# Optimization experiments

Hardware: AMD Instinct MI355X
Metric: run time of the kernel (lower is better)

Reference implementation:

```python
import jax, jax.numpy as jnp
import numpy as np

B, N, F, DEG = 64, 1024, 128, 8
K1, K2, K3 = 512, 256, 128  # ceil(0.5*N) cascaded pool sizes
NUM_CLASSES = 10
E = B * N * DEG

def _elu(x):
    return jnp.where(x > 0, x, jnp.expm1(x))

def gcn(x, W, b, src, dst, ev, n):
    # PyG GCNConv with improved=True: self-loop weight 2, symmetric norm
    h = x @ W
    w = ev.astype(h.dtype)
    deg = jax.ops.segment_sum(w, dst, num_segments=n) + 2.0
    dinv = jax.lax.rsqrt(deg)
    coef = (w * dinv[src] * dinv[dst])[:, None]
    out = jax.ops.segment_sum(h[src] * coef, dst, num_segments=n)
    out = out + h * (2.0 * dinv * dinv)[:, None]  # self-loop term
    return out + b

def topk_pool(x, p, src, dst, ev, bg, npg, k):
    # score = tanh(x.p/||p||); keep top-k per graph; mask+remap edges
    score = jnp.tanh((x @ p) / jnp.linalg.norm(p))
    vals, idx = jax.lax.top_k(score.reshape(bg, npg), k)
    perm = (idx + (jnp.arange(bg) * npg)[:, None]).reshape(-1)
    x_new = x[perm] * vals.reshape(-1)[:, None]
    remap = jnp.full((bg * npg,), -1, jnp.int32).at[perm].set(
        jnp.arange(bg * k, dtype=jnp.int32))
    s2, d2 = remap[src], remap[dst]
    ev2 = ev & (s2 >= 0) & (d2 >= 0)
    return x_new, jnp.maximum(s2, 0), jnp.maximum(d2, 0), ev2, perm

def setup_inputs() -> dict:
    key = jax.random.key(0)
    ks = jax.random.split(key, 16)
    offs = (jnp.arange(B) * N)[:, None]
    e_per = DEG * N
    src = (jax.random.randint(ks[0], (B, e_per), 0, N) + offs).reshape(-1).astype(jnp.int32)
    dst = (jax.random.randint(ks[1], (B, e_per), 0, N) + offs).reshape(-1).astype(jnp.int32)
    def w(k, shape, fan_in):
        return jax.random.normal(k, shape, jnp.float32) / np.sqrt(fan_in)
    return {
        "x": jax.random.normal(ks[2], (B * N, F), jnp.float32),
        "W1": w(ks[3], (F, 32), F), "b1": jnp.zeros((32,)), "p1": w(ks[4], (32,), 32),
        "W2": w(ks[5], (32, 64), 32), "b2": jnp.zeros((64,)), "p2": w(ks[6], (64,), 64),
        "W3": w(ks[7], (64, 128), 64), "b3": jnp.zeros((128,)), "p3": w(ks[8], (128,), 128),
        "W4": w(ks[9], (128, 256), 128), "b4": jnp.zeros((256,)),
        "W5": w(ks[10], (384, 128), 384), "b5": jnp.zeros((128,)),
        "W6": w(ks[11], (192, 64), 192), "b6": jnp.zeros((64,)),
        "W7": w(ks[12], (96, 32), 96), "b7": jnp.zeros((32,)),
        "Wl": w(ks[13], (64, 64), 64),
        "Wc": w(ks[14], (64, NUM_CLASSES), 64), "bc": jnp.zeros((NUM_CLASSES,)),
        "src": src, "dst": dst,
    }

def reference(x, W1, b1, p1, W2, b2, p2, W3, b3, p3, W4, b4,
              W5, b5, W6, b6, W7, b7, Wl, Wc, bc, src, dst):
    ev0 = jnp.ones((E,), bool)
    x1 = _elu(gcn(x, W1, b1, src, dst, ev0, B * N))
    x2, s2, d2, ev2, idx2 = topk_pool(x1, p1, src, dst, ev0, B, N, K1)
    x2 = _elu(x2)
    x3 = _elu(gcn(x2, W2, b2, s2, d2, ev2, B * K1))
    x4, s4, d4, ev4, idx4 = topk_pool(x3, p2, s2, d2, ev2, B, K1, K2)
    x4 = _elu(x4)
    x5 = _elu(gcn(x4, W3, b3, s4, d4, ev4, B * K2))
    x6, s6, d6, ev6, idx6 = topk_pool(x5, p3, s4, d4, ev4, B, K2, K3)
    x6 = _elu(x6)
    x7 = _elu(gcn(x6, W4, b4, s6, d6, ev6, B * K3))
    x8 = jnp.zeros((B * K2, 256), x7.dtype).at[idx6].set(x7)
    x8 = _elu(jnp.concatenate([x8, x5], axis=1))
    x9 = _elu(gcn(x8, W5, b5, s4, d4, ev4, B * K2))
    x10 = jnp.zeros((B * K1, 128), x9.dtype).at[idx4].set(x9)
    x10 = _elu(jnp.concatenate([x10, x3], axis=1))
    x11 = _elu(gcn(x10, W6, b6, s2, d2, ev2, B * K1))
    x12 = jnp.zeros((B * N, 64), x11.dtype).at[idx2].set(x11)
    x12 = _elu(jnp.concatenate([x12, x1], axis=1))
    x13 = _elu(gcn(x12, W7, b7, src, dst, ev0, B * N))
    batch = jnp.repeat(jnp.arange(B), N)
    gmp = jax.ops.segment_max(x13, batch, num_segments=B)
    gap = jax.ops.segment_sum(x13, batch, num_segments=B) / N
    g = _elu(jnp.concatenate([gmp, gap], axis=1))
    g = _elu(g @ Wl)
    logits = g @ Wc + bc
    return jax.nn.log_softmax(logits, axis=-1)
```

## Files before the change

kernel.cpp:

```cpp
#include <hip/hip_runtime.h>
#include <hip/hip_bf16.h>
#include <math.h>

#define B_ 64
#define N_ 1024
#define E_ 524288
#define K1_ 512
#define K2_ 256
#define K3_ 128
#define M0_ 65536
#define M1_ 32768
#define M2_ 16384
#define M3_ 8192

static __device__ __forceinline__ float eluf(float x){ return x > 0.f ? x : expm1f(x); }
static __device__ __forceinline__ float4 elu4(float4 v){
  float4 o; o.x=eluf(v.x); o.y=eluf(v.y); o.z=eluf(v.z); o.w=eluf(v.w); return o;
}

template<int BM,int BN,int MODE>
__global__ __launch_bounds__(256) void k_mm(const float* __restrict__ X,
    const float* __restrict__ W, float* __restrict__ H, int M, int K, int N,
    const int* __restrict__ perm, const float* __restrict__ vals,
    const float* __restrict__ Xd, const int* __restrict__ orig,
    const int* __restrict__ rm, int WD4){
  constexpr int TX = BN/4;
  constexpr int TY = 256/TX;
  constexpr int RM = BM/TY;
  __shared__ float Xs[BM][36];
  __shared__ float Ws[32][BN];
  const int t = threadIdx.x;
  const int tx = t % TX, ty = t / TX;
  const int m0 = blockIdx.x*BM, n0 = blockIdx.y*BN;
  float acc[RM][4];
  #pragma unroll
  for (int r=0;r<RM;++r){acc[r][0]=0.f;acc[r][1]=0.f;acc[r][2]=0.f;acc[r][3]=0.f;}
  for (int k0=0;k0<K;k0+=32){
    #pragma unroll
    for (int l=0;l<BM/32;++l){
      int fi=l*256+t, row=fi>>3, q=fi&7;
      int m = m0+row;
      int c4 = (k0>>2)+q;
      float4 v;
      if (MODE==0){
        v = *(const float4*)(X + (size_t)m*K + (c4<<2));
      } else if (MODE==1){
        int pm = perm[m]; float vv = vals[m];
        float4 h = *(const float4*)(X + (size_t)pm*K + (c4<<2));
        v.x=eluf(h.x*vv); v.y=eluf(h.y*vv); v.z=eluf(h.z*vv); v.w=eluf(h.w*vv);
      } else {
        if (c4 < WD4){
          int o = orig ? orig[m] : m;
          int j = rm[o];
          if (j>=0) v = elu4(*(const float4*)(Xd + ((size_t)j*WD4 + c4)*4));
          else { v.x=0.f;v.y=0.f;v.z=0.f;v.w=0.f; }
        } else {
          int ws4 = (K>>2) - WD4;
          v = elu4(*(const float4*)(X + ((size_t)m*ws4 + (c4-WD4))*4));
        }
      }
      *(float4*)(&Xs[row][q*4]) = v;
    }
    #pragma unroll
    for (int l=0;l<BN/32;++l){
      int fi=l*256+t, wrow=fi/(BN/4), wq=fi%(BN/4);
      *(float4*)(&Ws[wrow][wq*4]) = *(const float4*)(W + (size_t)(k0+wrow)*N + n0 + wq*4);
    }
    __syncthreads();
    #pragma unroll
    for (int kq=0;kq<32;kq+=4){
      float4 xv[RM];
      #pragma unroll
      for (int r=0;r<RM;++r) xv[r] = *(const float4*)(&Xs[ty*RM+r][kq]);
      #pragma unroll
      for (int j=0;j<4;++j){
        float4 wv = *(const float4*)(&Ws[kq+j][tx*4]);
        #pragma unroll
        for (int r=0;r<RM;++r){
          float xs = (j==0)?xv[r].x:(j==1)?xv[r].y:(j==2)?xv[r].z:xv[r].w;
          acc[r][0]=fmaf(xs,wv.x,acc[r][0]);
          acc[r][1]=fmaf(xs,wv.y,acc[r][1]);
          acc[r][2]=fmaf(xs,wv.z,acc[r][2]);
          acc[r][3]=fmaf(xs,wv.w,acc[r][3]);
        }
      }
    }
    __syncthreads();
  }
  #pragma unroll
  for (int r=0;r<RM;++r){
    int m = m0 + ty*RM + r;
    float4 h; h.x=acc[r][0];h.y=acc[r][1];h.z=acc[r][2];h.w=acc[r][3];
    *(float4*)(H + (size_t)m*N + n0 + tx*4) = h;
  }
}

__global__ void k_deg0(const int* __restrict__ dst, int* __restrict__ degi){
  int i = blockIdx.x*256+threadIdx.x; if (i>=E_) return;
  atomicAdd(&degi[dst[i]], 1);
}
__global__ void k_place0(const int* __restrict__ src, const int* __restrict__ dst,
                         int* __restrict__ cursor, int* __restrict__ col){
  int i = blockIdx.x*256+threadIdx.x; if (i>=E_) return;
  int p = atomicAdd(&cursor[dst[i]], 1);
  col[p] = src[i];
}

__global__ __launch_bounds__(256) void k_scanA(const int* __restrict__ degi,
                                               int* __restrict__ bsum){
  __shared__ int ls[256];
  int b = blockIdx.x, t = threadIdx.x;
  ls[t] = degi[b*256+t]; __syncthreads();
  for (int o=128;o>0;o>>=1){ if (t<o) ls[t]+=ls[t+o]; __syncthreads(); }
  if (t==0) bsum[b] = ls[0];
}
__global__ __launch_bounds__(256) void k_scanB(int* __restrict__ bsum){
  __shared__ int ps[256];
  int t = threadIdx.x;
  ps[t] = bsum[t]; __syncthreads();
  for (int o=1;o<256;o<<=1){
    int v = (t>=o) ? ps[t-o] : 0;
    __syncthreads(); ps[t]+=v; __syncthreads();
  }
  bsum[t] = ps[t];
}
__global__ __launch_bounds__(256) void k_scanC(const int* __restrict__ degi,
    const int* __restrict__ bsum, int* __restrict__ rowptr,
    int* __restrict__ cursor, float* __restrict__ dinv){
  __shared__ int ps[256];
  int b = blockIdx.x, t = threadIdx.x;
  int i = b*256+t;
  int d = degi[i];
  ps[t] = d; __syncthreads();
  for (int o=1;o<256;o<<=1){
    int v = (t>=o) ? ps[t-o] : 0;
    __syncthreads(); ps[t]+=v; __syncthreads();
  }
  int off = (b==0 ? 0 : bsum[b-1]) + ps[t] - d;
  rowptr[i] = off; cursor[i] = off;
  dinv[i] = rsqrtf((float)d + 2.f);
  if (i == M0_-1) rowptr[M0_] = off + d;
}

__global__ void k_deg_orig(const int* __restrict__ orig, const int* __restrict__ rowptr0,
                           const int* __restrict__ col0, const int* __restrict__ rm,
                           float* __restrict__ dinv, int M){
  int i = blockIdx.x*256+threadIdx.x; if (i>=M) return;
  int o = orig[i];
  int beg = rowptr0[o], end = rowptr0[o+1];
  int d = 0;
  for (int j=beg;j<end;++j) d += (rm[col0[j]] >= 0) ? 1 : 0;
  dinv[i] = rsqrtf((float)d + 2.f);
}

__global__ void k_compose_idx(const int* __restrict__ prevOrig, const int* __restrict__ idxL,
                              int* __restrict__ origL, int n){
  int i = blockIdx.x*256+threadIdx.x; if (i<n) origL[i] = prevOrig[idxL[i]];
}

template<int F, bool SCORE>
__global__ __launch_bounds__(256) void k_gather(const int* __restrict__ rowptr,
    const int* __restrict__ col, const float* __restrict__ dinv,
    const float* __restrict__ H, const float* __restrict__ bias,
    float* __restrict__ OUT, int M,
    const float* __restrict__ p, float* __restrict__ score){
  constexpr int FQ = F/4;
  int i = blockIdx.x*256+threadIdx.x;
  if (i >= M*FQ) return;
  int n = i/FQ, q = i - (i/FQ)*FQ;
  int beg = rowptr[n], end = rowptr[n+1];
  float4 acc; acc.x=0.f;acc.y=0.f;acc.z=0.f;acc.w=0.f;
  for (int j=beg;j<end;++j){
    int s = col[j];
    float c = dinv[s];
    float4 h = *(const float4*)(H + (size_t)s*F + q*4);
    acc.x=fmaf(c,h.x,acc.x); acc.y=fmaf(c,h.y,acc.y);
    acc.z=fmaf(c,h.z,acc.z); acc.w=fmaf(c,h.w,acc.w);
  }
  float dn = dinv[n];
  float sc = 2.f*dn*dn;
  float4 hn = *(const float4*)(H + (size_t)n*F + q*4);
  float4 bv = *(const float4*)(bias + q*4);
  float4 o;
  o.x = eluf(fmaf(sc,hn.x,fmaf(dn,acc.x,bv.x)));
  o.y = eluf(fmaf(sc,hn.y,fmaf(dn,acc.y,bv.y)));
  o.z = eluf(fmaf(sc,hn.z,fmaf(dn,acc.z,bv.z)));
  o.w = eluf(fmaf(sc,hn.w,fmaf(dn,acc.w,bv.w)));
  *(float4*)(OUT + (size_t)n*F + q*4) = o;
  if (SCORE){
    float4 pv = *(const float4*)(p + q*4);
    float dot = o.x*pv.x + o.y*pv.y + o.z*pv.z + o.w*pv.w;
    float n2  = pv.x*pv.x + pv.y*pv.y + pv.z*pv.z + pv.w*pv.w;
    #pragma unroll
    for (int mk=FQ>>1; mk>0; mk>>=1){
      dot += __shfl_xor(dot, mk);
      n2  += __shfl_xor(n2,  mk);
    }
    if (q==0) score[n] = tanhf(dot * rsqrtf(n2));
  }
}

template<int F, bool SCORE>
__global__ __launch_bounds__(256) void k_gather_rm(const int* __restrict__ orig,
    const int* __restrict__ rowptr0, const int* __restrict__ col0,
    const int* __restrict__ rm, const float* __restrict__ dinv,
    const float* __restrict__ H, const float* __restrict__ bias,
    float* __restrict__ OUT, int M,
    const float* __restrict__ p, float* __restrict__ score){
  constexpr int FQ = F/4;
  int i = blockIdx.x*256+threadIdx.x;
  if (i >= M*FQ) return;
  int n = i/FQ, q = i - (i/FQ)*FQ;
  int o = orig[n];
  int beg = rowptr0[o], end = rowptr0[o+1];
  float4 acc; acc.x=0.f;acc.y=0.f;acc.z=0.f;acc.w=0.f;
  for (int j=beg;j<end;++j){
    int s = rm[col0[j]];
    if (s >= 0){
      float c = dinv[s];
      float4 h = *(const float4*)(H + (size_t)s*F + q*4);
      acc.x=fmaf(c,h.x,acc.x); acc.y=fmaf(c,h.y,acc.y);
      acc.z=fmaf(c,h.z,acc.z); acc.w=fmaf(c,h.w,acc.w);
    }
  }
  float dn = dinv[n];
  float sc = 2.f*dn*dn;
  float4 hn = *(const float4*)(H + (size_t)n*F + q*4);
  float4 bv = *(const float4*)(bias + q*4);
  float4 ov;
  ov.x = eluf(fmaf(sc,hn.x,fmaf(dn,acc.x,bv.x)));
  ov.y = eluf(fmaf(sc,hn.y,fmaf(dn,acc.y,bv.y)));
  ov.z = eluf(fmaf(sc,hn.z,fmaf(dn,acc.z,bv.z)));
  ov.w = eluf(fmaf(sc,hn.w,fmaf(dn,acc.w,bv.w)));
  *(float4*)(OUT + (size_t)n*F + q*4) = ov;
  if (SCORE){
    float4 pv = *(const float4*)(p + q*4);
    float dot = ov.x*pv.x + ov.y*pv.y + ov.z*pv.z + ov.w*pv.w;
    float n2  = pv.x*pv.x + pv.y*pv.y + pv.z*pv.z + pv.w*pv.w;
    #pragma unroll
    for (int mk=FQ>>1; mk>0; mk>>=1){
      dot += __shfl_xor(dot, mk);
      n2  += __shfl_xor(n2,  mk);
    }
    if (q==0) score[n] = tanhf(dot * rsqrtf(n2));
  }
}

__global__ void k_topk(const float* __restrict__ score, int npg, int K,
                       int* __restrict__ perm, float* __restrict__ vals){
  __shared__ float ss[1024]; __shared__ int si[1024];
  int g = blockIdx.x, tid = threadIdx.x;
  ss[tid] = score[g*npg + tid]; si[tid] = tid;
  __syncthreads();
  for (int k=2;k<=npg;k<<=1){
    for (int j=k>>1;j>0;j>>=1){
      int ixj = tid ^ j;
      if (ixj > tid){
        float s1=ss[tid], s2=ss[ixj]; int i1=si[tid], i2=si[ixj];
        bool aAfterB = (s1 < s2) || (s1==s2 && i1 > i2);
        bool sw = ((tid & k)==0) ? aAfterB : !aAfterB;
        if (sw){ ss[tid]=s2; si[tid]=i2; ss[ixj]=s1; si[ixj]=i1; }
      }
      __syncthreads();
    }
  }
  if (tid < K){ perm[g*K+tid] = g*npg + si[tid]; vals[g*K+tid] = ss[tid]; }
}

__global__ void k_remap_set(const int* __restrict__ perm, int* __restrict__ remap, int n){
  int i = blockIdx.x*256+threadIdx.x; if (i<n) remap[perm[i]] = i;
}

__global__ void k_head(const float* __restrict__ x13, const float* __restrict__ Wl,
                       const float* __restrict__ Wc, const float* __restrict__ bc,
                       float* __restrict__ out){
  __shared__ float smax[256], ssum[256];
  __shared__ float gv[64], g2[64], logit[10];
  int g = blockIdx.x, t = threadIdx.x;
  int f = t & 31, r0 = t >> 5;
  float mx = -3.4e38f, sm = 0.f;
  const float* base = x13 + (size_t)g*N_*32;
  for (int r=r0; r<N_; r+=8){ float v = base[r*32+f]; mx = fmaxf(mx,v); sm += v; }
  smax[t]=mx; ssum[t]=sm; __syncthreads();
  if (t<128){ smax[t]=fmaxf(smax[t],smax[t+128]); ssum[t]+=ssum[t+128]; } __syncthreads();
  if (t<64){ smax[t]=fmaxf(smax[t],smax[t+64]); ssum[t]+=ssum[t+64]; } __syncthreads();
  if (t<32){
    float m2 = fmaxf(smax[t],smax[t+32]); float s2 = ssum[t]+ssum[t+32];
    gv[t] = eluf(m2); gv[32+t] = eluf(s2 * (1.f/N_));
  }
  __syncthreads();
  if (t<64){
    float acc=0.f;
    #pragma unroll
    for (int i2=0;i2<64;++i2) acc = fmaf(gv[i2], Wl[i2*64+t], acc);
    g2[t] = eluf(acc);
  }
  __syncthreads();
  if (t<10){
    float acc = bc[t];
    #pragma unroll
    for (int j=0;j<64;++j) acc = fmaf(g2[j], Wc[j*10+t], acc);
    logit[t] = acc;
  }
  __syncthreads();
  if (t==0){
    float m=-3.4e38f; for (int c=0;c<10;++c) m=fmaxf(m,logit[c]);
    float s=0.f; for (int c=0;c<10;++c) s += expf(logit[c]-m);
    float lse = m + logf(s);
    for (int c=0;c<10;++c) out[g*10+c] = logit[c]-lse;
  }
}

extern "C" void kernel_launch(void* const* d_in, const int* in_sizes, int n_in,
                              void* d_out, int out_size, void* d_ws, size_t ws_size,
                              hipStream_t stream){
  const float* x  = (const float*)d_in[0];
  const float* W1 = (const float*)d_in[1];
  const float* b1 = (const float*)d_in[2];
  const float* p1 = (const float*)d_in[3];
  const float* W2 = (const float*)d_in[4];
  const float* b2 = (const float*)d_in[5];
  const float* p2 = (const float*)d_in[6];
  const float* W3 = (const float*)d_in[7];
  const float* b3 = (const float*)d_in[8];
  const float* p3 = (const float*)d_in[9];
  const float* W4 = (const float*)d_in[10];
  const float* b4 = (const float*)d_in[11];
  const float* W5 = (const float*)d_in[12];
  const float* b5 = (const float*)d_in[13];
  const float* W6 = (const float*)d_in[14];
  const float* b6 = (const float*)d_in[15];
  const float* W7 = (const float*)d_in[16];
  const float* b7 = (const float*)d_in[17];
  const float* Wl = (const float*)d_in[18];
  const float* Wc = (const float*)d_in[19];
  const float* bc = (const float*)d_in[20];
  const int* src0 = (const int*)d_in[21];
  const int* dst0 = (const int*)d_in[22];
  float* out = (float*)d_out;

  char* wsp = (char*)d_ws;
  size_t off = 0;
  auto alloc = [&](size_t bytes)->char*{
    char* p = wsp + off;
    off += (bytes + 255) & ~(size_t)255;
    return p;
  };
  float* bufA = (float*)alloc((size_t)2097152*4);
  float* bufB = (float*)alloc((size_t)2097152*4);
  float* bufC = (float*)alloc((size_t)2097152*4);
  float* bufD = (float*)alloc((size_t)2097152*4);
  float* bufH = (float*)alloc((size_t)2097152*4);
  float* score= (float*)alloc((size_t)M0_*4);
  float* vals2= (float*)alloc((size_t)M1_*4);
  float* vals4= (float*)alloc((size_t)M2_*4);
  float* vals6= (float*)alloc((size_t)M3_*4);
  int* idx2 = (int*)alloc((size_t)M1_*4);
  int* idx4 = (int*)alloc((size_t)M2_*4);
  int* idx6 = (int*)alloc((size_t)M3_*4);
  int* orig4 = (int*)alloc((size_t)M2_*4);
  int* orig6 = (int*)alloc((size_t)M3_*4);
  int* rm02 = (int*)alloc((size_t)M0_*4);
  int* rm04 = (int*)alloc((size_t)M0_*4);
  int* rm06 = (int*)alloc((size_t)M0_*4);
  int* col0 = (int*)alloc((size_t)E_*4);
  int* rowptr0 = (int*)alloc((size_t)(M0_+1)*4);
  int* cursor0 = (int*)alloc((size_t)M0_*4);
  int* degi0 = (int*)alloc((size_t)M0_*4);
  int* bsum  = (int*)alloc((size_t)256*4);
  float* dinv0 = (float*)alloc((size_t)M0_*4);
  float* dinv2 = (float*)alloc((size_t)M1_*4);
  float* dinv4 = (float*)alloc((size_t)M2_*4);
  float* dinv6 = (float*)alloc((size_t)M3_*4);

  auto NB = [](int total){ return (total+255)/256; };

  hipMemsetAsync(degi0, 0, (size_t)M0_*4, stream);
  k_deg0<<<NB(E_),256,0,stream>>>(dst0, degi0);
  k_scanA<<<256,256,0,stream>>>(degi0, bsum);
  k_scanB<<<1,256,0,stream>>>(bsum);
  k_scanC<<<256,256,0,stream>>>(degi0, bsum, rowptr0, cursor0, dinv0);
  k_place0<<<NB(E_),256,0,stream>>>(src0, dst0, cursor0, col0);

  k_mm<128,32,0><<<dim3(M0_/128,1),256,0,stream>>>(x, W1, bufH, M0_, 128, 32,
      nullptr,nullptr,nullptr,nullptr,nullptr,0);
  k_gather<32,true><<<NB(M0_*8),256,0,stream>>>(rowptr0, col0, dinv0, bufH, b1, bufA, M0_, p1, score);

  k_topk<<<B_,1024,0,stream>>>(score, 1024, K1_, idx2, vals2);
  hipMemsetAsync(rm02, 0xFF, (size_t)M0_*4, stream);
  k_remap_set<<<NB(M1_),256,0,stream>>>(idx2, rm02, M1_);
  k_deg_orig<<<NB(M1_),256,0,stream>>>(idx2, rowptr0, col0, rm02, dinv2, M1_);

  k_mm<64,64,1><<<dim3(M1_/64,1),256,0,stream>>>(bufA, W2, bufH, M1_, 32, 64,
      idx2, vals2, nullptr,nullptr,nullptr,0);
  k_gather_rm<64,true><<<NB(M1_*16),256,0,stream>>>(idx2, rowptr0, col0, rm02, dinv2, bufH, b2, bufB, M1_, p2, score);

  k_topk<<<B_,512,0,stream>>>(score, 512, K2_, idx4, vals4);
  k_compose_idx<<<NB(M2_),256,0,stream>>>(idx2, idx4, orig4, M2_);
  hipMemsetAsync(rm04, 0xFF, (size_t)M0_*4, stream);
  k_remap_set<<<NB(M2_),256,0,stream>>>(orig4, rm04, M2_);
  k_deg_orig<<<NB(M2_),256,0,stream>>>(orig4, rowptr0, col0, rm04, dinv4, M2_);

  k_mm<64,64,1><<<dim3(M2_/64,2),256,0,stream>>>(bufB, W3, bufH, M2_, 64, 128,
      idx4, vals4, nullptr,nullptr,nullptr,0);
  k_gather_rm<128,true><<<NB(M2_*32),256,0,stream>>>(orig4, rowptr0, col0, rm04, dinv4, bufH, b3, bufC, M2_, p3, score);

  k_topk<<<B_,256,0,stream>>>(score, 256, K3_, idx6, vals6);
  k_compose_idx<<<NB(M3_),256,0,stream>>>(orig4, idx6, orig6, M3_);
  hipMemsetAsync(rm06, 0xFF, (size_t)M0_*4, stream);
  k_remap_set<<<NB(M3_),256,0,stream>>>(orig6, rm06, M3_);
  k_deg_orig<<<NB(M3_),256,0,stream>>>(orig6, rowptr0, col0, rm06, dinv6, M3_);

  k_mm<64,64,1><<<dim3(M3_/64,4),256,0,stream>>>(bufC, W4, bufH, M3_, 128, 256,
      idx6, vals6, nullptr,nullptr,nullptr,0);
  k_gather_rm<256,false><<<NB(M3_*64),256,0,stream>>>(orig6, rowptr0, col0, rm06, dinv6, bufH, b4, bufD, M3_, nullptr, nullptr);

  k_mm<64,64,2><<<dim3(M2_/64,2),256,0,stream>>>(bufC, W5, bufH, M2_, 384, 128,
      nullptr,nullptr, bufD, orig4, rm06, 64);
  k_gather_rm<128,false><<<NB(M2_*32),256,0,stream>>>(orig4, rowptr0, col0, rm04, dinv4, bufH, b5, bufD, M2_, nullptr, nullptr);

  k_mm<64,64,2><<<dim3(M1_/64,1),256,0,stream>>>(bufB, W6, bufH, M1_, 192, 64,
      nullptr,nullptr, bufD, idx2, rm04, 32);
  k_gather_rm<64,false><<<NB(M1_*16),256,0,stream>>>(idx2, rowptr0, col0, rm02, dinv2, bufH, b6, bufC, M1_, nullptr, nullptr);

  k_mm<128,32,2><<<dim3(M0_/128,1),256,0,stream>>>(bufA, W7, bufH, M0_, 96, 32,
      nullptr,nullptr, bufC, nullptr, rm02, 16);
  k_gather<32,false><<<NB(M0_*8),256,0,stream>>>(rowptr0, col0, dinv0, bufH, b7, bufA, M0_, nullptr, nullptr);

  k_head<<<B_,256,0,stream>>>(bufA, Wl, Wc, bc, out);

  (void)in_sizes; (void)n_in; (void)out_size; (void)ws_size;
}
```

Before: 403.9 us.

## Build CSR per graph in one kernel and fuse top-k pooling bookkeeping

Replaces the global degree-count, three-pass scan and edge-placement kernels with a single per-graph kernel that counts degrees, scans and places edges using shared-memory atomics. This relies on edges being grouped by graph in contiguous blocks of 8192. It also fuses top-k sorting, index composition, remap reset and set, and pooled degree computation into one kernel per pooling level. The aim is to remove many small kernel launches, memsets and global atomics. In exchange the CSR and pooling work run on only 64 blocks, and correctness depends on the edge-ordering assumption and on the remap writes being visible within each block.

```diff
diff --git a/kernel.cpp b/kernel.cpp
--- a/kernel.cpp
+++ b/kernel.cpp
@@ -5,6 +5,7 @@
 #define B_ 64
 #define N_ 1024
 #define E_ 524288
+#define EPG_ 8192
 #define K1_ 512
 #define K2_ 256
 #define K3_ 128
@@ -95,67 +96,81 @@
   }
 }
 
-__global__ void k_deg0(const int* __restrict__ dst, int* __restrict__ degi){
-  int i = blockIdx.x*256+threadIdx.x; if (i>=E_) return;
-  atomicAdd(&degi[dst[i]], 1);
-}
-__global__ void k_place0(const int* __restrict__ src, const int* __restrict__ dst,
-                         int* __restrict__ cursor, int* __restrict__ col){
-  int i = blockIdx.x*256+threadIdx.x; if (i>=E_) return;
-  int p = atomicAdd(&cursor[dst[i]], 1);
-  col[p] = src[i];
-}
-
-__global__ __launch_bounds__(256) void k_scanA(const int* __restrict__ degi,
-                                               int* __restrict__ bsum){
-  __shared__ int ls[256];
-  int b = blockIdx.x, t = threadIdx.x;
-  ls[t] = degi[b*256+t]; __syncthreads();
-  for (int o=128;o>0;o>>=1){ if (t<o) ls[t]+=ls[t+o]; __syncthreads(); }
-  if (t==0) bsum[b] = ls[0];
-}
-__global__ __launch_bounds__(256) void k_scanB(int* __restrict__ bsum){
-  __shared__ int ps[256];
-  int t = threadIdx.x;
-  ps[t] = bsum[t]; __syncthreads();
-  for (int o=1;o<256;o<<=1){
+__global__ __launch_bounds__(1024) void k_csr(const int* __restrict__ src0,
+    const int* __restrict__ dst0, int* __restrict__ rowptr,
+    int* __restrict__ col, float* __restrict__ dinv){
+  __shared__ int ldeg[1024];
+  __shared__ int ps[1024];
+  __shared__ int lcur[1024];
+  const int g = blockIdx.x, t = threadIdx.x;
+  const int ebase = g*EPG_, nbase = g<<10;
+  ldeg[t] = 0;
+  __syncthreads();
+  #pragma unroll
+  for (int i=0;i<EPG_/1024;++i){
+    int e = ebase + i*1024 + t;
+    atomicAdd(&ldeg[dst0[e] - nbase], 1);
+  }
+  __syncthreads();
+  int d = ldeg[t];
+  ps[t] = d; __syncthreads();
+  for (int o=1;o<1024;o<<=1){
     int v = (t>=o) ? ps[t-o] : 0;
-    __syncthreads(); ps[t]+=v; __syncthreads();
-  }
-  bsum[t] = ps[t];
-}
-__global__ __launch_bounds__(256) void k_scanC(const int* __restrict__ degi,
-    const int* __restrict__ bsum, int* __restrict__ rowptr,
-    int* __restrict__ cursor, float* __restrict__ dinv){
-  __shared__ int ps[256];
-  int b = blockIdx.x, t = threadIdx.x;
-  int i = b*256+t;
-  int d = degi[i];
-  ps[t] = d; __syncthreads();
-  for (int o=1;o<256;o<<=1){
-    int v = (t>=o) ? ps[t-o] : 0;
-    __syncthreads(); ps[t]+=v; __syncthreads();
-  }
-  int off = (b==0 ? 0 : bsum[b-1]) + ps[t] - d;
-  rowptr[i] = off; cursor[i] = off;
-  dinv[i] = rsqrtf((float)d + 2.f);
-  if (i == M0_-1) rowptr[M0_] = off + d;
-}
-
-__global__ void k_deg_orig(const int* __restrict__ orig, const int* __restrict__ rowptr0,
-                           const int* __restrict__ col0, const int* __restrict__ rm,
-                           float* __restrict__ dinv, int M){
-  int i = blockIdx.x*256+threadIdx.x; if (i>=M) return;
-  int o = orig[i];
-  int beg = rowptr0[o], end = rowptr0[o+1];
-  int d = 0;
-  for (int j=beg;j<end;++j) d += (rm[col0[j]] >= 0) ? 1 : 0;
-  dinv[i] = rsqrtf((float)d + 2.f);
-}
-
-__global__ void k_compose_idx(const int* __restrict__ prevOrig, const int* __restrict__ idxL,
-                              int* __restrict__ origL, int n){
-  int i = blockIdx.x*256+threadIdx.x; if (i<n) origL[i] = prevOrig[idxL[i]];
+    __syncthreads(); ps[t] += v; __syncthreads();
+  }
+  int excl = ps[t] - d;
+  rowptr[nbase + t] = ebase + excl;
+  lcur[t] = excl;
+  dinv[nbase + t] = rsqrtf((float)d + 2.f);
+  if (g == B_-1 && t == 1023) rowptr[M0_] = E_;
+  __syncthreads();
+  #pragma unroll
+  for (int i=0;i<EPG_/1024;++i){
+    int e = ebase + i*1024 + t;
+    int dl = dst0[e] - nbase;
+    int p = atomicAdd(&lcur[dl], 1);
+    col[ebase + p] = src0[e];
+  }
+}
+
+__global__ __launch_bounds__(1024) void k_pool(const float* __restrict__ score,
+    int npg, int K, const int* __restrict__ prevOrig,
+    const int* __restrict__ rowptr0, const int* __restrict__ col0,
+    int* __restrict__ perm, float* __restrict__ vals,
+    int* __restrict__ orig, int* __restrict__ rm, float* __restrict__ dinv){
+  __shared__ float ss[1024]; __shared__ int si[1024];
+  const int g = blockIdx.x, t = threadIdx.x;
+  for (int i=t; i<1024; i+=npg) rm[(g<<10)+i] = -1;
+  ss[t] = score[g*npg + t]; si[t] = t;
+  __syncthreads();
+  for (int k=2;k<=npg;k<<=1){
+    for (int j=k>>1;j>0;j>>=1){
+      int ixj = t ^ j;
+      if (ixj > t){
+        float s1=ss[t], s2=ss[ixj]; int i1=si[t], i2=si[ixj];
+        bool aAfterB = (s1 < s2) || (s1==s2 && i1 > i2);
+        bool sw = ((t & k)==0) ? aAfterB : !aAfterB;
+        if (sw){ ss[t]=s2; si[t]=i2; ss[ixj]=s1; si[ixj]=i1; }
+      }
+      __syncthreads();
+    }
+  }
+  int o = -1;
+  if (t < K){
+    int pl = g*npg + si[t];
+    perm[g*K+t] = pl;
+    vals[g*K+t] = ss[t];
+    o = prevOrig ? prevOrig[pl] : pl;
+    orig[g*K+t] = o;
+    rm[o] = g*K + t;
+  }
+  __syncthreads();
+  if (t < K){
+    int beg = rowptr0[o], end = rowptr0[o+1];
+    int d = 0;
+    for (int j=beg;j<end;++j) d += (rm[col0[j]] >= 0) ? 1 : 0;
+    dinv[g*K+t] = rsqrtf((float)d + 2.f);
+  }
 }
 
 template<int F, bool SCORE>
@@ -244,31 +259,6 @@
     }
     if (q==0) score[n] = tanhf(dot * rsqrtf(n2));
   }
-}
-
-__global__ void k_topk(const float* __restrict__ score, int npg, int K,
-                       int* __restrict__ perm, float* __restrict__ vals){
-  __shared__ float ss[1024]; __shared__ int si[1024];
-  int g = blockIdx.x, tid = threadIdx.x;
-  ss[tid] = score[g*npg + tid]; si[tid] = tid;
-  __syncthreads();
-  for (int k=2;k<=npg;k<<=1){
-    for (int j=k>>1;j>0;j>>=1){
-      int ixj = tid ^ j;
-      if (ixj > tid){
-        float s1=ss[tid], s2=ss[ixj]; int i1=si[tid], i2=si[ixj];
-        bool aAfterB = (s1 < s2) || (s1==s2 && i1 > i2);
-        bool sw = ((tid & k)==0) ? aAfterB : !aAfterB;
-        if (sw){ ss[tid]=s2; si[tid]=i2; ss[ixj]=s1; si[ixj]=i1; }
-      }
-      __syncthreads();
-    }
-  }
-  if (tid < K){ perm[g*K+tid] = g*npg + si[tid]; vals[g*K+tid] = ss[tid]; }
-}
-
-__global__ void k_remap_set(const int* __restrict__ perm, int* __restrict__ remap, int n){
-  int i = blockIdx.x*256+threadIdx.x; if (i<n) remap[perm[i]] = i;
 }
 
 __global__ void k_head(const float* __restrict__ x13, const float* __restrict__ Wl,
@@ -365,9 +355,6 @@
   int* rm06 = (int*)alloc((size_t)M0_*4);
   int* col0 = (int*)alloc((size_t)E_*4);
   int* rowptr0 = (int*)alloc((size_t)(M0_+1)*4);
-  int* cursor0 = (int*)alloc((size_t)M0_*4);
-  int* degi0 = (int*)alloc((size_t)M0_*4);
-  int* bsum  = (int*)alloc((size_t)256*4);
   float* dinv0 = (float*)alloc((size_t)M0_*4);
   float* dinv2 = (float*)alloc((size_t)M1_*4);
   float* dinv4 = (float*)alloc((size_t)M2_*4);
@@ -375,41 +362,28 @@
 
   auto NB = [](int total){ return (total+255)/256; };
 
-  hipMemsetAsync(degi0, 0, (size_t)M0_*4, stream);
-  k_deg0<<<NB(E_),256,0,stream>>>(dst0, degi0);
-  k_scanA<<<256,256,0,stream>>>(degi0, bsum);
-  k_scanB<<<1,256,0,stream>>>(bsum);
-  k_scanC<<<256,256,0,stream>>>(degi0, bsum, rowptr0, cursor0, dinv0);
-  k_place0<<<NB(E_),256,0,stream>>>(src0, dst0, cursor0, col0);
+  k_csr<<<B_,1024,0,stream>>>(src0, dst0, rowptr0, col0, dinv0);
 
   k_mm<128,32,0><<<dim3(M0_/128,1),256,0,stream>>>(x, W1, bufH, M0_, 128, 32,
       nullptr,nullptr,nullptr,nullptr,nullptr,0);
   k_gather<32,true><<<NB(M0_*8),256,0,stream>>>(rowptr0, col0, dinv0, bufH, b1, bufA, M0_, p1, score);
 
-  k_topk<<<B_,1024,0,stream>>>(score, 1024, K1_, idx2, vals2);
-  hipMemsetAsync(rm02, 0xFF, (size_t)M0_*4, stream);
-  k_remap_set<<<NB(M1_),256,0,stream>>>(idx2, rm02, M1_);
-  k_deg_orig<<<NB(M1_),256,0,stream>>>(idx2, rowptr0, col0, rm02, dinv2, M1_);
+  k_pool<<<B_,1024,0,stream>>>(score, 1024, K1_, nullptr, rowptr0, col0,
+      idx2, vals2, idx2, rm02, dinv2);
 
   k_mm<64,64,1><<<dim3(M1_/64,1),256,0,stream>>>(bufA, W2, bufH, M1_, 32, 64,
       idx2, vals2, nullptr,nullptr,nullptr,0);
   k_gather_rm<64,true><<<NB(M1_*16),256,0,stream>>>(idx2, rowptr0, col0, rm02, dinv2, bufH, b2, bufB, M1_, p2, score);
 
-  k_topk<<<B_,512,0,stream>>>(score, 512, K2_, idx4, vals4);
-  k_compose_idx<<<NB(M2_),256,0,stream>>>(idx2, idx4, orig4, M2_);
-  hipMemsetAsync(rm04, 0xFF, (size_t)M0_*4, stream);
-  k_remap_set<<<NB(M2_),256,0,stream>>>(orig4, rm04, M2_);
-  k_deg_orig<<<NB(M2_),256,0,stream>>>(orig4, rowptr0, col0, rm04, dinv4, M2_);
+  k_pool<<<B_,512,0,stream>>>(score, 512, K2_, idx2, rowptr0, col0,
+      idx4, vals4, orig4, rm04, dinv4);
 
   k_mm<64,64,1><<<dim3(M2_/64,2),256,0,stream>>>(bufB, W3, bufH, M2_, 64, 128,
       idx4, vals4, nullptr,nullptr,nullptr,0);
   k_gather_rm<128,true><<<NB(M2_*32),256,0,stream>>>(orig4, rowptr0, col0, rm04, dinv4, bufH, b3, bufC, M2_, p3, score);
 
-  k_topk<<<B_,256,0,stream>>>(score, 256, K3_, idx6, vals6);
-  k_compose_idx<<<NB(M3_),256,0,stream>>>(orig4, idx6, orig6, M3_);
-  hipMemsetAsync(rm06, 0xFF, (size_t)M0_*4, stream);
-  k_remap_set<<<NB(M3_),256,0,stream>>>(orig6, rm06, M3_);
-  k_deg_orig<<<NB(M3_),256,0,stream>>>(orig6, rowptr0, col0, rm06, dinv6, M3_);
+  k_pool<<<B_,256,0,stream>>>(score, 256, K3_, orig4, rowptr0, col0,
+      idx6, vals6, orig6, rm06, dinv6);
 
   k_mm<64,64,1><<<dim3(M3_/64,4),256,0,stream>>>(bufC, W4, bufH, M3_, 128, 256,
       idx6, vals6, nullptr,nullptr,nullptr,0);
```

After: 349.7 us. 1.15x faster.
